# Performance work log

Hardware: AMD Instinct MI355X
Metric: run time of the kernel (lower is better)

The kernel has to match this reference:

```python
import jax, jax.numpy as jnp
import numpy as np

NH = 8
D_MODEL = 512
D_K = D_MODEL // NH
B, S = 2, 4096


def setup_inputs() -> dict:
    key = jax.random.key(0)
    ks = jax.random.split(key, 8)
    scale = 1.0 / np.sqrt(D_MODEL)
    return {
        "query": jax.random.normal(ks[0], (B, S, D_MODEL), dtype=jnp.float32),
        "key": jax.random.normal(ks[1], (B, S, D_MODEL), dtype=jnp.float32),
        "value": jax.random.normal(ks[2], (B, S, D_MODEL), dtype=jnp.float32),
        "mask": jax.random.randint(ks[3], (B, 1, S, S), 0, 2) > 0,
        "Wq": jax.random.normal(ks[4], (D_MODEL, D_MODEL), dtype=jnp.float32) * scale,
        "Wk": jax.random.normal(ks[5], (D_MODEL, D_MODEL), dtype=jnp.float32) * scale,
        "Wv": jax.random.normal(ks[6], (D_MODEL, D_MODEL), dtype=jnp.float32) * scale,
        "Wo": jax.random.normal(ks[7], (D_MODEL, D_MODEL), dtype=jnp.float32) * scale,
    }


def reference(query, key, value, mask, Wq, Wk, Wv, Wo):
    # Linear (no bias): torch Linear stores W as [out, in], y = x @ W^T.
    def proj(x, W):
        # [B, S, D] -> [B, nh, S, d_k]
        y = jnp.einsum("bsd,ed->bse", x, W)
        return y.reshape(B, S, NH, D_K).transpose(0, 2, 1, 3)

    q = proj(query, Wq)
    k = proj(key, Wk)
    v = proj(value, Wv)

    scores = jnp.einsum("bhqd,bhkd->bhqk", q, k) / jnp.sqrt(jnp.float32(D_K))
    scores = jnp.where(mask, jnp.float32(-1e9), scores)
    p_attn = jax.nn.softmax(scores, axis=-1)
    x = jnp.einsum("bhqk,bhkd->bhqd", p_attn, v)  # [B, nh, S, d_k]
    x = x.transpose(0, 2, 1, 3).reshape(B, S, D_MODEL)
    return jnp.einsum("bsd,ed->bse", x, Wo)
```

## Files before the change

kernel.cpp:

```cpp
#include <hip/hip_runtime.h>


#define S_LEN   4096
#define DM      512
#define NHEAD   8
#define DKH     64
#define NT      (S_LEN / 64)
#define NEG_BIG (-1e9f)
#define MINIT   (-3.402823466e38f)

typedef __bf16 bf16x8 __attribute__((ext_vector_type(8)));
typedef __bf16 bf16x4 __attribute__((ext_vector_type(4)));
typedef float  f32x4  __attribute__((ext_vector_type(4)));
typedef unsigned long long u64;

__device__ inline void gload_lds16(const void* g, void* l) {
    __builtin_amdgcn_global_load_lds(
        (const __attribute__((address_space(1))) unsigned int*)g,
        (__attribute__((address_space(3))) unsigned int*)l, 16, 0, 0);
}

__device__ inline uint4 cvt8(float4 a, float4 b) {
    union { bf16x8 v; uint4 u; } c;
    c.v[0] = (__bf16)a.x; c.v[1] = (__bf16)a.y;
    c.v[2] = (__bf16)a.z; c.v[3] = (__bf16)a.w;
    c.v[4] = (__bf16)b.x; c.v[5] = (__bf16)b.y;
    c.v[6] = (__bf16)b.z; c.v[7] = (__bf16)b.w;
    return c.u;
}

__global__ __launch_bounds__(256)
void cast_w(const float* __restrict__ Wq, const float* __restrict__ Wk,
            const float* __restrict__ Wv, const float* __restrict__ Wo,
            __bf16* __restrict__ out)
{
    const int t = blockIdx.x * 256 + threadIdx.x;
    const int e = t * 8;
    const int z = e >> 18;
    const int i = e & 262143;
    const float* W = (z == 0) ? Wq : (z == 1) ? Wk : (z == 2) ? Wv : Wo;
    const float4 a = *(const float4*)&W[i];
    const float4 b = *(const float4*)&W[i + 4];
    *(uint4*)&out[e] = cvt8(a, b);
}

__global__ __launch_bounds__(256)
void pack_mask(const int* __restrict__ m, u64* __restrict__ bits)
{
    const size_t i = (size_t)blockIdx.x * 256 + threadIdx.x;
    const u64 b = __ballot(m[i] != 0);
    if ((threadIdx.x & 63) == 0) bits[i >> 6] = b;
}

template<int MODE>
__global__ __launch_bounds__(512, 4)
void gemm_mfma(const float* __restrict__ X0, const float* __restrict__ X1,
               const float* __restrict__ X2, const __bf16* __restrict__ Xb,
               const __bf16* __restrict__ Wb,
               __bf16* __restrict__ Y0, __bf16* __restrict__ Y1,
               __bf16* __restrict__ Y2, float* __restrict__ Yf)
{
    __shared__ __align__(16) char lds[32768];
    char* Xs = lds;
    char* Ws = lds + 16384;

    const int tid  = threadIdx.x;
    const int lane = tid & 63;
    const int l15  = lane & 15;
    const int lhi  = lane >> 4;
    const int w    = tid >> 6;
    const int wr   = w >> 2;
    const int wc   = w & 3;
    const int row0 = blockIdx.x << 7;
    const int col0 = blockIdx.y << 7;
    const int z    = blockIdx.z;

    const float*  Xf = (z == 0) ? X0 : (z == 1) ? X1 : X2;
    __bf16*       Yb = (z == 0) ? Y0 : (z == 1) ? Y1 : Y2;
    const __bf16* W  = Wb + (size_t)(MODE == 0 ? z : 0) * DM * DM;

    const int sr = tid >> 2;
    const int sc = (tid & 3) << 1;

    f32x4 acc[4][2];
    #pragma unroll
    for (int m = 0; m < 4; ++m)
        #pragma unroll
        for (int n = 0; n < 2; ++n)
            acc[m][n] = (f32x4){0.f, 0.f, 0.f, 0.f};

    for (int k0 = 0; k0 < DM; k0 += 64) {
        uint4 xa, xb2;
        if (MODE == 0) {
            const size_t base = (size_t)(row0 + sr) * DM + k0 + sc * 8;
            const float4 a0 = *(const float4*)&Xf[base];
            const float4 a1 = *(const float4*)&Xf[base + 4];
            const float4 a2 = *(const float4*)&Xf[base + 8];
            const float4 a3 = *(const float4*)&Xf[base + 12];
            xa = cvt8(a0, a1); xb2 = cvt8(a2, a3);
        }
        __syncthreads();
        if (MODE == 0) {
            *(uint4*)(Xs + sr * 128 + ((sc       ^ (sr & 7)) << 4)) = xa;
            *(uint4*)(Xs + sr * 128 + (((sc + 1) ^ (sr & 7)) << 4)) = xb2;
        } else {
            #pragma unroll
            for (int s = 0; s < 2; ++s) {
                const int f = w * 128 + s * 64 + lane;
                const int r = f >> 3, sl = f & 7;
                gload_lds16(&Xb[(size_t)(row0 + r) * DM + k0 + ((sl ^ (r & 7)) << 3)],
                            Xs + w * 2048 + s * 1024);
            }
        }
        #pragma unroll
        for (int s = 0; s < 2; ++s) {
            const int f = w * 128 + s * 64 + lane;
            const int r = f >> 3, sl = f & 7;
            gload_lds16(&W[(size_t)(col0 + r) * DM + k0 + ((sl ^ (r & 7)) << 3)],
                        Ws + w * 2048 + s * 1024);
        }
        __syncthreads();

        #pragma unroll
        for (int kk = 0; kk < 2; ++kk) {
            bf16x8 xf[4], wf[2];
            #pragma unroll
            for (int m = 0; m < 4; ++m) {
                const int r = wr * 64 + m * 16 + l15;
                xf[m] = *(const bf16x8*)(Xs + r * 128 + ((((kk << 2) + lhi) ^ (r & 7)) << 4));
            }
            #pragma unroll
            for (int n = 0; n < 2; ++n) {
                const int r = wc * 32 + n * 16 + l15;
                wf[n] = *(const bf16x8*)(Ws + r * 128 + ((((kk << 2) + lhi) ^ (r & 7)) << 4));
            }
            #pragma unroll
            for (int m = 0; m < 4; ++m)
                #pragma unroll
                for (int n = 0; n < 2; ++n)
                    acc[m][n] = __builtin_amdgcn_mfma_f32_16x16x32_bf16(wf[n], xf[m], acc[m][n], 0, 0, 0);
        }
    }

    const float osc = (MODE == 0 && z == 0) ? 0.125f : 1.0f;
    #pragma unroll
    for (int m = 0; m < 4; ++m) {
        const int r = row0 + wr * 64 + m * 16 + l15;
        #pragma unroll
        for (int n = 0; n < 2; ++n) {
            const int cb = col0 + wc * 32 + n * 16 + lhi * 4;
            if (MODE == 0) {
                bf16x4 o4;
                o4[0] = (__bf16)(acc[m][n][0] * osc);
                o4[1] = (__bf16)(acc[m][n][1] * osc);
                o4[2] = (__bf16)(acc[m][n][2] * osc);
                o4[3] = (__bf16)(acc[m][n][3] * osc);
                const int bb = r >> 12, srow = r & 4095;
                const int hh = cb >> 6, dk = cb & 63;
                *(bf16x4*)&Yb[(((size_t)(bb * NHEAD + hh)) * S_LEN + srow) * DKH + dk] = o4;
            } else {
                *(float4*)&Yf[(size_t)r * DM + cb] = *(float4*)&acc[m][n];
            }
        }
    }
}

__global__ __launch_bounds__(512, 4)
void attn_mfma(const __bf16* __restrict__ Q, const __bf16* __restrict__ K,
               const __bf16* __restrict__ V, const u64* __restrict__ bits,
               __bf16* __restrict__ ctx)
{
    __shared__ __align__(16) char lds[49152];

    const int tid  = threadIdx.x;
    const int lane = tid & 63;
    const int w    = tid >> 6;
    const int l15  = lane & 15;
    const int lhi  = lane >> 4;
    const int q0   = blockIdx.x << 7;
    const int h    = blockIdx.y;
    const int b    = blockIdx.z;

    const __bf16* Qb = Q + (size_t)(b * NHEAD + h) * S_LEN * DKH;
    const __bf16* Kb = K + (size_t)(b * NHEAD + h) * S_LEN * DKH;
    const __bf16* Vb = V + (size_t)(b * NHEAD + h) * S_LEN * DKH;

    const int qrow = q0 + w * 16 + l15;
    const u64* Mb = bits + (size_t)b * (S_LEN * (S_LEN / 64)) + (size_t)qrow * 64;

    const bf16x8 qa0 = *(const bf16x8*)&Qb[(size_t)qrow * DKH + lhi * 8];
    const bf16x8 qa1 = *(const bf16x8*)&Qb[(size_t)qrow * DKH + 32 + lhi * 8];

    char* psb = lds + 32768 + w * 2048;

    f32x4 o[4];
    float m_r = MINIT, l_r = 0.f;
    #pragma unroll
    for (int dt = 0; dt < 4; ++dt) o[dt] = (f32x4){0.f, 0.f, 0.f, 0.f};

    const int krow = tid >> 3, kslot = tid & 7;
    const int vj   = tid & 63, vd0 = (tid >> 6) * 8;

    gload_lds16(&Kb[(size_t)krow * DKH + ((kslot ^ (krow & 7)) << 3)],
                lds + w * 1024);
    {
        const uint4 v0 = *(const uint4*)&Vb[(size_t)vj * DKH + vd0];
        char* Vt = lds + 8192;
        const __bf16* vr = (const __bf16*)&v0;
        #pragma unroll
        for (int i = 0; i < 8; ++i) {
            const int d = vd0 + i;
            *(__bf16*)(Vt + ((d * 128 + vj * 2) ^ ((d & 7) << 4))) = vr[i];
        }
    }
    u64 mcur = Mb[0];
    __syncthreads();

    for (int t = 0; t < NT; ++t) {
        const int c  = t & 1;
        const int tn = (t + 1 < NT) ? (t + 1) : t;

        gload_lds16(&Kb[(size_t)((tn << 6) + krow) * DKH + ((kslot ^ (krow & 7)) << 3)],
                    lds + (c ^ 1) * 16384 + w * 1024);
        const uint4 vnxt = *(const uint4*)&Vb[(size_t)((tn << 6) + vj) * DKH + vd0];
        const u64   mnxt = Mb[tn];

        const char* Ksb = lds + c * 16384;
        const char* Vtb = Ksb + 8192;

        f32x4 s[4];
        __builtin_amdgcn_s_setprio(1);
        #pragma unroll
        for (int tt = 0; tt < 4; ++tt) {
            const int kr  = tt * 16 + l15;
            const int off = kr * 128 + ((lhi ^ (kr & 7)) << 4);
            const bf16x8 kb0 = *(const bf16x8*)(Ksb + off);
            const bf16x8 kb1 = *(const bf16x8*)(Ksb + (off ^ 64));
            f32x4 zz = (f32x4){0.f, 0.f, 0.f, 0.f};
            zz    = __builtin_amdgcn_mfma_f32_16x16x32_bf16(kb0, qa0, zz, 0, 0, 0);
            s[tt] = __builtin_amdgcn_mfma_f32_16x16x32_bf16(kb1, qa1, zz, 0, 0, 0);
        }
        __builtin_amdgcn_s_setprio(0);

        const unsigned int lo = (unsigned int)mcur, hi = (unsigned int)(mcur >> 32);
        unsigned int shf[4];
        shf[0] = lo >> (lhi << 2);
        shf[1] = lo >> (16 + (lhi << 2));
        shf[2] = hi >> (lhi << 2);
        shf[3] = hi >> (16 + (lhi << 2));

        float pv[4][4];
        #pragma unroll
        for (int tt = 0; tt < 4; ++tt)
            #pragma unroll
            for (int r = 0; r < 4; ++r)
                pv[tt][r] = ((shf[tt] >> r) & 1) ? NEG_BIG : s[tt][r];

        float tmax = pv[0][0];
        #pragma unroll
        for (int tt = 0; tt < 4; ++tt)
            #pragma unroll
            for (int r = 0; r < 4; ++r)
                tmax = fmaxf(tmax, pv[tt][r]);
        tmax = fmaxf(tmax, __shfl_xor(tmax, 16));
        tmax = fmaxf(tmax, __shfl_xor(tmax, 32));

        if (!__all(tmax <= m_r + 8.f)) {
            const float newm  = fmaxf(m_r, tmax);
            const float alpha = __expf(m_r - newm);
            m_r = newm;
            l_r *= alpha;
            #pragma unroll
            for (int dt = 0; dt < 4; ++dt) {
                o[dt][0] *= alpha; o[dt][1] *= alpha;
                o[dt][2] *= alpha; o[dt][3] *= alpha;
            }
        }

        float rsum = 0.f;
        #pragma unroll
        for (int tt = 0; tt < 4; ++tt)
            #pragma unroll
            for (int r = 0; r < 4; ++r) {
                pv[tt][r] = __expf(pv[tt][r] - m_r);
                rsum += pv[tt][r];
            }
        rsum += __shfl_xor(rsum, 16);
        rsum += __shfl_xor(rsum, 32);
        l_r += rsum;

        #pragma unroll
        for (int tt = 0; tt < 4; ++tt)
            #pragma unroll
            for (int cc = 0; cc < 2; ++cc) {
                union { __bf16 h2[2]; unsigned int u; } pk;
                pk.h2[0] = (__bf16)pv[tt][2 * cc];
                pk.h2[1] = (__bf16)pv[tt][2 * cc + 1];
                const int kbyte = tt * 32 + (lhi << 3) + (cc << 2);
                const int off = l15 * 128
                              + (((kbyte >> 4) ^ (l15 & 7)) << 4) + (kbyte & 15);
                *(unsigned int*)(psb + off) = pk.u;
            }
        const int poff = l15 * 128 + ((lhi ^ (l15 & 7)) << 4);
        const bf16x8 pb0 = *(const bf16x8*)(psb + poff);
        const bf16x8 pb1 = *(const bf16x8*)(psb + (poff ^ 64));

        __builtin_amdgcn_s_setprio(1);
        #pragma unroll
        for (int dt = 0; dt < 4; ++dt) {
            const int vrow = dt * 16 + l15;
            const int voff = vrow * 128 + ((lhi ^ (vrow & 7)) << 4);
            const bf16x8 vb0 = *(const bf16x8*)(Vtb + voff);
            const bf16x8 vb1 = *(const bf16x8*)(Vtb + (voff ^ 64));
            o[dt] = __builtin_amdgcn_mfma_f32_16x16x32_bf16(vb0, pb0, o[dt], 0, 0, 0);
            o[dt] = __builtin_amdgcn_mfma_f32_16x16x32_bf16(vb1, pb1, o[dt], 0, 0, 0);
        }
        __builtin_amdgcn_s_setprio(0);

        {
            char* Vt = lds + (c ^ 1) * 16384 + 8192;
            const __bf16* vr = (const __bf16*)&vnxt;
            #pragma unroll
            for (int i = 0; i < 8; ++i) {
                const int d = vd0 + i;
                *(__bf16*)(Vt + ((d * 128 + vj * 2) ^ ((d & 7) << 4))) = vr[i];
            }
        }
        __syncthreads();
        mcur = mnxt;
    }

    const float inv = 1.f / l_r;
    #pragma unroll
    for (int dt = 0; dt < 4; ++dt) {
        bf16x4 ov;
        ov[0] = (__bf16)(o[dt][0] * inv);
        ov[1] = (__bf16)(o[dt][1] * inv);
        ov[2] = (__bf16)(o[dt][2] * inv);
        ov[3] = (__bf16)(o[dt][3] * inv);
        *(bf16x4*)&ctx[((size_t)b * S_LEN + qrow) * DM + h * DKH + dt * 16 + lhi * 4] = ov;
    }
}

extern "C" void kernel_launch(void* const* d_in, const int* in_sizes, int n_in,
                              void* d_out, int out_size, void* d_ws, size_t ws_size,
                              hipStream_t stream)
{
    const float* q    = (const float*)d_in[0];
    const float* k    = (const float*)d_in[1];
    const float* v    = (const float*)d_in[2];
    const int*   mask = (const int*)d_in[3];
    const float* Wq   = (const float*)d_in[4];
    const float* Wk   = (const float*)d_in[5];
    const float* Wv   = (const float*)d_in[6];
    const float* Wo   = (const float*)d_in[7];
    float* out = (float*)d_out;

    const size_t per = (size_t)2 * S_LEN * DM;
    __bf16* wb   = (__bf16*)d_ws;
    __bf16* Qh   = wb + (size_t)4 * DM * DM;
    __bf16* Kh   = Qh + per;
    __bf16* Vh   = Kh + per;
    __bf16* ctx  = Vh + per;
    u64*    bits = (u64*)(ctx + per);

    cast_w<<<dim3(512), dim3(256), 0, stream>>>(Wq, Wk, Wv, Wo, wb);

    pack_mask<<<dim3((2 * S_LEN * S_LEN) / 256), dim3(256), 0, stream>>>(mask, bits);

    gemm_mfma<0><<<dim3(64, 4, 3), dim3(512), 0, stream>>>(
        q, k, v, nullptr, wb, Qh, Kh, Vh, nullptr);

    attn_mfma<<<dim3(S_LEN / 128, NHEAD, 2), dim3(512), 0, stream>>>(
        Qh, Kh, Vh, bits, ctx);

    gemm_mfma<1><<<dim3(64, 4, 1), dim3(512), 0, stream>>>(
        nullptr, nullptr, nullptr, ctx, wb + (size_t)3 * DM * DM,
        nullptr, nullptr, nullptr, out);
}
```

Before: 420.4 us.

## Fuse prep kernels, pre-cast inputs, double-buffer GEMM, transpose mask bits, exp2 softmax

Merges the weight cast and mask packing into a single prep kernel that also casts q/k/v to bf16. The projection GEMM can then load both operands straight into LDS via double-buffered global_load_lds with MFMA priority hints. Mask bits are stored transposed so each query row's bits for a key tile are contiguous across lanes, and the attention grid is remapped to interleave blocks across XCDs. Softmax switches to exp2 with log2e folded into the Q scale, uses a tree max and writes P with wider packed stores. The extra fp32-to-bf16 pass over the inputs adds memory traffic, and the LDS usage of the GEMM doubles.

Result: slower. 440.2 us (+4.7%).

```diff
diff --git a/kernel.cpp b/kernel.cpp
--- a/kernel.cpp
+++ b/kernel.cpp
@@ -6,13 +6,17 @@
 #define NHEAD   8
 #define DKH     64
 #define NT      (S_LEN / 64)
-#define NEG_BIG (-1e9f)
+#define LOG2E   1.44269504088896f
+#define NEG2    (-1.44269504e9f)
 #define MINIT   (-3.402823466e38f)
+#define QSCALE  (0.125f * LOG2E)
 
 typedef __bf16 bf16x8 __attribute__((ext_vector_type(8)));
 typedef __bf16 bf16x4 __attribute__((ext_vector_type(4)));
 typedef float  f32x4  __attribute__((ext_vector_type(4)));
 typedef unsigned long long u64;
+
+#define F3(a,b,c) fmaxf(fmaxf((a),(b)),(c))
 
 __device__ inline void gload_lds16(const void* g, void* l) {
     __builtin_amdgcn_global_load_lds(
@@ -30,39 +34,55 @@
 }
 
 __global__ __launch_bounds__(256)
-void cast_w(const float* __restrict__ Wq, const float* __restrict__ Wk,
-            const float* __restrict__ Wv, const float* __restrict__ Wo,
-            __bf16* __restrict__ out)
+void prep(const float* __restrict__ q, const float* __restrict__ k,
+          const float* __restrict__ v, const int* __restrict__ mask,
+          const float* __restrict__ Wq, const float* __restrict__ Wk,
+          const float* __restrict__ Wv, const float* __restrict__ Wo,
+          __bf16* __restrict__ wb, __bf16* __restrict__ xb,
+          u64* __restrict__ bits)
 {
-    const int t = blockIdx.x * 256 + threadIdx.x;
-    const int e = t * 8;
-    const int z = e >> 18;
-    const int i = e & 262143;
-    const float* W = (z == 0) ? Wq : (z == 1) ? Wk : (z == 2) ? Wv : Wo;
-    const float4 a = *(const float4*)&W[i];
-    const float4 b = *(const float4*)&W[i + 4];
-    *(uint4*)&out[e] = cvt8(a, b);
-}
-
-__global__ __launch_bounds__(256)
-void pack_mask(const int* __restrict__ m, u64* __restrict__ bits)
-{
-    const size_t i = (size_t)blockIdx.x * 256 + threadIdx.x;
-    const u64 b = __ballot(m[i] != 0);
-    if ((threadIdx.x & 63) == 0) bits[i >> 6] = b;
+    __shared__ u64 sm[4][64];
+    const int blk = blockIdx.x, tid = threadIdx.x;
+
+    if (blk < 512) {
+        const int t = blk * 256 + tid;
+        const int e = t * 8, z = e >> 18, i = e & 262143;
+        const float* W = (z == 0) ? Wq : (z == 1) ? Wk : (z == 2) ? Wv : Wo;
+        const float4 a = *(const float4*)&W[i];
+        const float4 b = *(const float4*)&W[i + 4];
+        *(uint4*)&wb[e] = cvt8(a, b);
+    } else if (blk < 6656) {
+        const int t = (blk - 512) * 256 + tid;
+        const int e = t * 8, z = e >> 22, i = e & 4194303;
+        const float* X = (z == 0) ? q : (z == 1) ? k : v;
+        const float4 a = *(const float4*)&X[i];
+        const float4 b = *(const float4*)&X[i + 4];
+        *(uint4*)&xb[e] = cvt8(a, b);
+    } else {
+        const int w4 = tid >> 6, lane = tid & 63;
+        const int gw = (blk - 6656) * 4 + w4;
+        const int p  = gw >> 6;
+        const int r0 = (gw & 63) << 6;
+        const int bb = p >> 6, wc = p & 63;
+        #pragma unroll 4
+        for (int it = 0; it < 64; ++it) {
+            const int r = r0 + it;
+            const size_t idx = (((size_t)(bb * S_LEN + r)) << 12) + (wc << 6) + lane;
+            const u64 bal = __ballot(mask[idx] != 0);
+            if (lane == 0) sm[w4][it] = bal;
+        }
+        bits[((size_t)p << 12) + r0 + lane] = sm[w4][lane];
+    }
 }
 
 template<int MODE>
 __global__ __launch_bounds__(512, 4)
-void gemm_mfma(const float* __restrict__ X0, const float* __restrict__ X1,
-               const float* __restrict__ X2, const __bf16* __restrict__ Xb,
-               const __bf16* __restrict__ Wb,
+void gemm_mfma(const __bf16* __restrict__ X0, const __bf16* __restrict__ X1,
+               const __bf16* __restrict__ X2, const __bf16* __restrict__ Wb,
                __bf16* __restrict__ Y0, __bf16* __restrict__ Y1,
                __bf16* __restrict__ Y2, float* __restrict__ Yf)
 {
-    __shared__ __align__(16) char lds[32768];
-    char* Xs = lds;
-    char* Ws = lds + 16384;
+    __shared__ __align__(16) char lds[65536];
 
     const int tid  = threadIdx.x;
     const int lane = tid & 63;
@@ -75,12 +95,8 @@
     const int col0 = blockIdx.y << 7;
     const int z    = blockIdx.z;
 
-    const float*  Xf = (z == 0) ? X0 : (z == 1) ? X1 : X2;
-    __bf16*       Yb = (z == 0) ? Y0 : (z == 1) ? Y1 : Y2;
-    const __bf16* W  = Wb + (size_t)(MODE == 0 ? z : 0) * DM * DM;
-
-    const int sr = tid >> 2;
-    const int sc = (tid & 3) << 1;
+    const __bf16* X = (z == 0) ? X0 : (z == 1) ? X1 : X2;
+    const __bf16* W = Wb + (size_t)(MODE == 0 ? z : 3) * DM * DM;
 
     f32x4 acc[4][2];
     #pragma unroll
@@ -89,38 +105,28 @@
         for (int n = 0; n < 2; ++n)
             acc[m][n] = (f32x4){0.f, 0.f, 0.f, 0.f};
 
-    for (int k0 = 0; k0 < DM; k0 += 64) {
-        uint4 xa, xb2;
-        if (MODE == 0) {
-            const size_t base = (size_t)(row0 + sr) * DM + k0 + sc * 8;
-            const float4 a0 = *(const float4*)&Xf[base];
-            const float4 a1 = *(const float4*)&Xf[base + 4];
-            const float4 a2 = *(const float4*)&Xf[base + 8];
-            const float4 a3 = *(const float4*)&Xf[base + 12];
-            xa = cvt8(a0, a1); xb2 = cvt8(a2, a3);
-        }
-        __syncthreads();
-        if (MODE == 0) {
-            *(uint4*)(Xs + sr * 128 + ((sc       ^ (sr & 7)) << 4)) = xa;
-            *(uint4*)(Xs + sr * 128 + (((sc + 1) ^ (sr & 7)) << 4)) = xb2;
-        } else {
-            #pragma unroll
-            for (int s = 0; s < 2; ++s) {
-                const int f = w * 128 + s * 64 + lane;
-                const int r = f >> 3, sl = f & 7;
-                gload_lds16(&Xb[(size_t)(row0 + r) * DM + k0 + ((sl ^ (r & 7)) << 3)],
-                            Xs + w * 2048 + s * 1024);
-            }
-        }
+    auto stage = [&](int c, int k0) {
+        char* Xs = lds + c * 32768;
+        char* Ws = Xs + 16384;
         #pragma unroll
         for (int s = 0; s < 2; ++s) {
             const int f = w * 128 + s * 64 + lane;
             const int r = f >> 3, sl = f & 7;
-            gload_lds16(&W[(size_t)(col0 + r) * DM + k0 + ((sl ^ (r & 7)) << 3)],
-                        Ws + w * 2048 + s * 1024);
-        }
-        __syncthreads();
-
+            const size_t go = (size_t)r * DM + k0 + ((sl ^ (r & 7)) << 3);
+            gload_lds16(&X[(size_t)row0 * DM + go], Xs + w * 2048 + s * 1024);
+            gload_lds16(&W[(size_t)col0 * DM + go], Ws + w * 2048 + s * 1024);
+        }
+    };
+
+    stage(0, 0);
+    __syncthreads();
+
+    for (int t = 0; t < 8; ++t) {
+        const int c = t & 1;
+        if (t < 7) stage(c ^ 1, (t + 1) * 64);
+
+        const char* Xs = lds + c * 32768;
+        const char* Ws = Xs + 16384;
         #pragma unroll
         for (int kk = 0; kk < 2; ++kk) {
             bf16x8 xf[4], wf[2];
@@ -134,15 +140,18 @@
                 const int r = wc * 32 + n * 16 + l15;
                 wf[n] = *(const bf16x8*)(Ws + r * 128 + ((((kk << 2) + lhi) ^ (r & 7)) << 4));
             }
+            __builtin_amdgcn_s_setprio(1);
             #pragma unroll
             for (int m = 0; m < 4; ++m)
                 #pragma unroll
                 for (int n = 0; n < 2; ++n)
                     acc[m][n] = __builtin_amdgcn_mfma_f32_16x16x32_bf16(wf[n], xf[m], acc[m][n], 0, 0, 0);
-        }
-    }
-
-    const float osc = (MODE == 0 && z == 0) ? 0.125f : 1.0f;
+            __builtin_amdgcn_s_setprio(0);
+        }
+        __syncthreads();
+    }
+
+    const float osc = (MODE == 0 && z == 0) ? QSCALE : 1.0f;
     #pragma unroll
     for (int m = 0; m < 4; ++m) {
         const int r = row0 + wr * 64 + m * 16 + l15;
@@ -157,6 +166,7 @@
                 o4[3] = (__bf16)(acc[m][n][3] * osc);
                 const int bb = r >> 12, srow = r & 4095;
                 const int hh = cb >> 6, dk = cb & 63;
+                __bf16* Yb = (z == 0) ? Y0 : (z == 1) ? Y1 : Y2;
                 *(bf16x4*)&Yb[(((size_t)(bb * NHEAD + hh)) * S_LEN + srow) * DKH + dk] = o4;
             } else {
                 *(float4*)&Yf[(size_t)r * DM + cb] = *(float4*)&acc[m][n];
@@ -177,16 +187,19 @@
     const int w    = tid >> 6;
     const int l15  = lane & 15;
     const int lhi  = lane >> 4;
-    const int q0   = blockIdx.x << 7;
-    const int h    = blockIdx.y;
-    const int b    = blockIdx.z;
+
+    const int d  = blockIdx.x;
+    const int wk = ((d & 7) << 6) + (d >> 3);
+    const int q0 = (wk & 31) << 7;
+    const int h  = (wk >> 5) & 7;
+    const int b  = wk >> 8;
 
     const __bf16* Qb = Q + (size_t)(b * NHEAD + h) * S_LEN * DKH;
     const __bf16* Kb = K + (size_t)(b * NHEAD + h) * S_LEN * DKH;
     const __bf16* Vb = V + (size_t)(b * NHEAD + h) * S_LEN * DKH;
 
     const int qrow = q0 + w * 16 + l15;
-    const u64* Mb = bits + (size_t)b * (S_LEN * (S_LEN / 64)) + (size_t)qrow * 64;
+    const u64* Mb = bits + ((size_t)b << 18) + qrow;
 
     const bf16x8 qa0 = *(const bf16x8*)&Qb[(size_t)qrow * DKH + lhi * 8];
     const bf16x8 qa1 = *(const bf16x8*)&Qb[(size_t)qrow * DKH + 32 + lhi * 8];
@@ -209,8 +222,8 @@
         const __bf16* vr = (const __bf16*)&v0;
         #pragma unroll
         for (int i = 0; i < 8; ++i) {
-            const int d = vd0 + i;
-            *(__bf16*)(Vt + ((d * 128 + vj * 2) ^ ((d & 7) << 4))) = vr[i];
+            const int dd = vd0 + i;
+            *(__bf16*)(Vt + ((dd * 128 + vj * 2) ^ ((dd & 7) << 4))) = vr[i];
         }
     }
     u64 mcur = Mb[0];
@@ -223,7 +236,7 @@
         gload_lds16(&Kb[(size_t)((tn << 6) + krow) * DKH + ((kslot ^ (krow & 7)) << 3)],
                     lds + (c ^ 1) * 16384 + w * 1024);
         const uint4 vnxt = *(const uint4*)&Vb[(size_t)((tn << 6) + vj) * DKH + vd0];
-        const u64   mnxt = Mb[tn];
+        const u64   mnxt = Mb[(size_t)tn << 12];
 
         const char* Ksb = lds + c * 16384;
         const char* Vtb = Ksb + 8192;
@@ -254,20 +267,20 @@
         for (int tt = 0; tt < 4; ++tt)
             #pragma unroll
             for (int r = 0; r < 4; ++r)
-                pv[tt][r] = ((shf[tt] >> r) & 1) ? NEG_BIG : s[tt][r];
-
-        float tmax = pv[0][0];
-        #pragma unroll
-        for (int tt = 0; tt < 4; ++tt)
-            #pragma unroll
-            for (int r = 0; r < 4; ++r)
-                tmax = fmaxf(tmax, pv[tt][r]);
+                pv[tt][r] = ((shf[tt] >> r) & 1) ? NEG2 : s[tt][r];
+
+        float a0 = F3(pv[0][0], pv[0][1], pv[0][2]);
+        float a1 = F3(pv[0][3], pv[1][0], pv[1][1]);
+        float a2 = F3(pv[1][2], pv[1][3], pv[2][0]);
+        float a3 = F3(pv[2][1], pv[2][2], pv[2][3]);
+        float a4 = F3(pv[3][0], pv[3][1], pv[3][2]);
+        float tmax = fmaxf(F3(a0, a1, a2), F3(a3, a4, pv[3][3]));
         tmax = fmaxf(tmax, __shfl_xor(tmax, 16));
         tmax = fmaxf(tmax, __shfl_xor(tmax, 32));
 
         if (!__all(tmax <= m_r + 8.f)) {
             const float newm  = fmaxf(m_r, tmax);
-            const float alpha = __expf(m_r - newm);
+            const float alpha = exp2f(m_r - newm);
             m_r = newm;
             l_r *= alpha;
             #pragma unroll
@@ -282,7 +295,7 @@
         for (int tt = 0; tt < 4; ++tt)
             #pragma unroll
             for (int r = 0; r < 4; ++r) {
-                pv[tt][r] = __expf(pv[tt][r] - m_r);
+                pv[tt][r] = exp2f(pv[tt][r] - m_r);
                 rsum += pv[tt][r];
             }
         rsum += __shfl_xor(rsum, 16);
@@ -290,17 +303,17 @@
         l_r += rsum;
 
         #pragma unroll
-        for (int tt = 0; tt < 4; ++tt)
-            #pragma unroll
-            for (int cc = 0; cc < 2; ++cc) {
-                union { __bf16 h2[2]; unsigned int u; } pk;
-                pk.h2[0] = (__bf16)pv[tt][2 * cc];
-                pk.h2[1] = (__bf16)pv[tt][2 * cc + 1];
-                const int kbyte = tt * 32 + (lhi << 3) + (cc << 2);
-                const int off = l15 * 128
-                              + (((kbyte >> 4) ^ (l15 & 7)) << 4) + (kbyte & 15);
-                *(unsigned int*)(psb + off) = pk.u;
-            }
+        for (int tt = 0; tt < 4; ++tt) {
+            union { __bf16 h2[4]; uint2 u; } pk;
+            pk.h2[0] = (__bf16)pv[tt][0];
+            pk.h2[1] = (__bf16)pv[tt][1];
+            pk.h2[2] = (__bf16)pv[tt][2];
+            pk.h2[3] = (__bf16)pv[tt][3];
+            const int off = l15 * 128
+                          + ((((tt << 1) + (lhi >> 1)) ^ (l15 & 7)) << 4)
+                          + ((lhi & 1) << 3);
+            *(uint2*)(psb + off) = pk.u;
+        }
         const int poff = l15 * 128 + ((lhi ^ (l15 & 7)) << 4);
         const bf16x8 pb0 = *(const bf16x8*)(psb + poff);
         const bf16x8 pb1 = *(const bf16x8*)(psb + (poff ^ 64));
@@ -322,8 +335,8 @@
             const __bf16* vr = (const __bf16*)&vnxt;
             #pragma unroll
             for (int i = 0; i < 8; ++i) {
-                const int d = vd0 + i;
-                *(__bf16*)(Vt + ((d * 128 + vj * 2) ^ ((d & 7) << 4))) = vr[i];
+                const int dd = vd0 + i;
+                *(__bf16*)(Vt + ((dd * 128 + vj * 2) ^ ((dd & 7) << 4))) = vr[i];
             }
         }
         __syncthreads();
@@ -358,23 +371,21 @@
 
     const size_t per = (size_t)2 * S_LEN * DM;
     __bf16* wb   = (__bf16*)d_ws;
-    __bf16* Qh   = wb + (size_t)4 * DM * DM;
+    __bf16* xb   = wb + (size_t)4 * DM * DM;
+    __bf16* Qh   = xb + 3 * per;
     __bf16* Kh   = Qh + per;
     __bf16* Vh   = Kh + per;
     __bf16* ctx  = Vh + per;
     u64*    bits = (u64*)(ctx + per);
 
-    cast_w<<<dim3(512), dim3(256), 0, stream>>>(Wq, Wk, Wv, Wo, wb);
-
-    pack_mask<<<dim3((2 * S_LEN * S_LEN) / 256), dim3(256), 0, stream>>>(mask, bits);
+    prep<<<dim3(8704), dim3(256), 0, stream>>>(q, k, v, mask,
+                                               Wq, Wk, Wv, Wo, wb, xb, bits);
 
     gemm_mfma<0><<<dim3(64, 4, 3), dim3(512), 0, stream>>>(
-        q, k, v, nullptr, wb, Qh, Kh, Vh, nullptr);
-
-    attn_mfma<<<dim3(S_LEN / 128, NHEAD, 2), dim3(512), 0, stream>>>(
-        Qh, Kh, Vh, bits, ctx);
+        xb, xb + per, xb + 2 * per, wb, Qh, Kh, Vh, nullptr);
+
+    attn_mfma<<<dim3(512), dim3(512), 0, stream>>>(Qh, Kh, Vh, bits, ctx);
 
     gemm_mfma<1><<<dim3(64, 4, 1), dim3(512), 0, stream>>>(
-        nullptr, nullptr, nullptr, ctx, wb + (size_t)3 * DM * DM,
-        nullptr, nullptr, nullptr, out);
-}
+        ctx, ctx, ctx, wb, nullptr, nullptr, nullptr, out);
+}
```
